# Kernel tuning notes

Measured on AMD Instinct MI355X. Metric: run time of the kernel, lower is better.

The kernel has to match this reference:

```python
import jax, jax.numpy as jnp
import numpy as np

W_LEN = 37  # window_length
EPS = 1e-9
LRELU_SLOPE = 0.2
SQRT2 = 1.4142135623730951


def win_sum(x, w):
    # Depthwise sliding-window sum of width w, 'same' padding w//2 (odd w).
    # Equivalent to the diag-kernel conv1d in the original code, but O(T) via cumsum.
    pad = w // 2
    xp = jnp.pad(x, ((0, 0), (0, 0), (pad, pad)))
    cs = jnp.cumsum(xp, axis=-1)
    cs = jnp.pad(cs, ((0, 0), (0, 0), (1, 0)))
    return cs[..., w:] - cs[..., :-w]


def conv1d(x, w, b):
    # x: [B,C,T], w: [O,I,3], padding=1
    y = jax.lax.conv_general_dilated(x, w, (1,), [(1, 1)],
                                     dimension_numbers=('NCH', 'OIH', 'NCH'))
    return y + b[None, :, None]


def adawin_instance(x, s, mask, fc_w, fc_b, alpha):
    # x: [B,C,T], s: [B,S,T], mask: [B,T]
    C = x.shape[1]
    h = jnp.einsum('bst,cs->bct', s, fc_w) + fc_b[None, :, None]  # [B,2C,T]
    m = mask[:, None, :]                       # [B,1,T]
    denom = win_sum(m, W_LEN) + EPS            # same for all channels
    gamma = win_sum(h[:, :C], W_LEN) / denom * m
    beta = win_sum(h[:, C:], W_LEN) / denom * m
    x_norm = jnp.tanh(alpha * x)               # WindowedNorm1d.forward
    return (1.0 + gamma) * x_norm + beta


def setup_inputs() -> dict:
    key = jax.random.key(0)
    ks = jax.random.split(key, 10)
    B, C_IN, C_OUT, S, T = 16, 512, 512, 128, 2048
    inp = {
        'x': jax.random.normal(ks[0], (B, C_IN, T), dtype=jnp.float32),
        's': jax.random.normal(ks[1], (B, S, T), dtype=jnp.float32),
        'lengths': jax.random.randint(ks[2], (B,), 0, T).astype(jnp.int32),
        'fc1_w': jax.random.normal(ks[3], (2 * C_IN, S), dtype=jnp.float32) * 0.05,
        'fc1_b': jnp.zeros((2 * C_IN,), dtype=jnp.float32),
        'alpha1': jnp.full((1,), 0.5, dtype=jnp.float32),
        'conv1_w': jax.random.normal(ks[4], (C_OUT, C_IN, 3), dtype=jnp.float32) * 0.02,
        'conv1_b': jnp.zeros((C_OUT,), dtype=jnp.float32),
        'fc2_w': jax.random.normal(ks[5], (2 * C_OUT, S), dtype=jnp.float32) * 0.05,
        'fc2_b': jnp.zeros((2 * C_OUT,), dtype=jnp.float32),
        'alpha2': jnp.full((1,), 0.5, dtype=jnp.float32),
        'conv2_w': jax.random.normal(ks[6], (C_OUT, C_OUT, 3), dtype=jnp.float32) * 0.02,
        'conv2_b': jnp.zeros((C_OUT,), dtype=jnp.float32),
    }
    return inp


def reference(x, s, lengths, fc1_w, fc1_b, alpha1, conv1_w, conv1_b,
              fc2_w, fc2_b, alpha2, conv2_w, conv2_b):
    T = x.shape[2]
    mask = (jnp.arange(T)[None, :] < lengths[:, None]).astype(x.dtype)  # [B,T]

    h = adawin_instance(x, s, mask, fc1_w, fc1_b, alpha1)
    h = jax.nn.leaky_relu(h, LRELU_SLOPE)
    h = conv1d(h, conv1_w, conv1_b)
    h = adawin_instance(h, s, mask, fc2_w, fc2_b, alpha2)
    h = jax.nn.leaky_relu(h, LRELU_SLOPE)
    h = conv1d(h, conv2_w, conv2_b)

    # dim_in == dim_out -> identity shortcut
    return (h + x) / SQRT2
```

## Files before the change

### kernel.cpp

```cpp
#include <hip/hip_runtime.h>

#define B_ 16
#define C_ 512
#define S_ 128
#define T_ 2048
#define HALF 18
#define WLEN 37

typedef __bf16 bf16x8 __attribute__((ext_vector_type(8)));
typedef float f32x4 __attribute__((ext_vector_type(4)));
typedef float f32x16 __attribute__((ext_vector_type(16)));
typedef unsigned short ushort_t;

__device__ inline ushort_t f2bf(float x) {
    unsigned u = __float_as_uint(x);
    u += 0x7fffu + ((u >> 16) & 1u);
    return (ushort_t)(u >> 16);
}
__device__ inline float bf2f(ushort_t h) {
    return __uint_as_float(((unsigned)h) << 16);
}

#define MFMA16(a, b, c) __builtin_amdgcn_mfma_f32_16x16x32_bf16((a), (b), (c), 0, 0, 0)
#define MFMA32(a, b, c) __builtin_amdgcn_mfma_f32_32x32x16_bf16((a), (b), (c), 0, 0, 0)

__global__ void prep_weights(const float* __restrict__ fc1, const float* __restrict__ fc2,
                             const float* __restrict__ c1, const float* __restrict__ c2,
                             ushort_t* __restrict__ Wfc, ushort_t* __restrict__ Wc1,
                             ushort_t* __restrict__ Wc2) {
    const int n_fc = 1024 * 128;
    const int n_c = 512 * 1536;
    const int total = 2 * n_fc + 2 * n_c;
    for (int idx = blockIdx.x * blockDim.x + threadIdx.x; idx < total;
         idx += gridDim.x * blockDim.x) {
        if (idx < n_fc) {
            Wfc[idx] = f2bf(fc1[idx]);
        } else if (idx < 2 * n_fc) {
            Wfc[idx] = f2bf(fc2[idx - n_fc]);
        } else {
            int r = idx - 2 * n_fc;
            const float* src = c1;
            ushort_t* dst = Wc1;
            if (r >= n_c) { r -= n_c; src = c2; dst = Wc2; }
            int o = r / 1536;
            int rem = r - o * 1536;
            int k = rem >> 9;
            int i = rem & 511;
            dst[o * 1536 + (k << 9) + i] = f2bf(src[(o * 512 + i) * 3 + k]);
        }
    }
}

__global__ void zero_pads(ushort_t* __restrict__ y1p, ushort_t* __restrict__ y2p) {
    int tid = blockIdx.x * blockDim.x + threadIdx.x;
    if (tid < 4096) {
        ushort_t* base = (tid & 1) ? y2p : y1p;
        int r = tid >> 1;
        int bb = r >> 7;
        int rowsel = (r >> 6) & 1;
        int col = (r & 63) * 8;
        size_t row = (size_t)bb * (T_ + 2) + (rowsel ? (T_ + 1) : 0);
        *(uint4*)&base[row * C_ + col] = (uint4){0, 0, 0, 0};
    }
}

__global__ __launch_bounds__(256) void winsum_kernel(const float* __restrict__ s,
                                                     ushort_t* __restrict__ sw_t) {
    int b = blockIdx.y;
    int t0 = blockIdx.x * 64;
    __shared__ float sb[128][101];
    int tid = threadIdx.x;
    for (int e = tid; e < 128 * 100; e += 256) {
        int sj = e / 100;
        int u = e - sj * 100;
        int gt = t0 - HALF + u;
        float v = 0.f;
        if (gt >= 0 && gt < T_) v = s[((size_t)(b * S_ + sj)) * T_ + gt];
        sb[sj][u] = v;
    }
    __syncthreads();
    for (int e = tid; e < 64 * 128; e += 256) {
        int tl = e >> 7;
        int sj = e & 127;
        float sum = 0.f;
#pragma unroll
        for (int d = 0; d < WLEN; ++d) sum += sb[sj][tl + d];
        sw_t[((size_t)(b * T_ + t0 + tl)) * S_ + sj] = f2bf(sum);
    }
}

template <int INLAYOUT>
__global__ __launch_bounds__(256) void adawin_kernel(
    const void* __restrict__ xin_, const ushort_t* __restrict__ sw_t,
    const ushort_t* __restrict__ Wfc, const float* __restrict__ fcb,
    const float* __restrict__ alpha, const int* __restrict__ lengths,
    ushort_t* __restrict__ youtp) {
    int t0 = blockIdx.x * 64;
    int c0 = blockIdx.y * 64;
    int b = blockIdx.z;
    __shared__ __attribute__((aligned(16))) ushort_t As[128][136];
    __shared__ __attribute__((aligned(16))) ushort_t Bs[64][136];
    int tid = threadIdx.x;

    {
        int r = tid >> 4;
        int cseg = (tid & 15) * 8;
#pragma unroll
        for (int p = 0; p < 8; ++p) {
            int row = p * 16 + r;
            int grow = (row < 64) ? (c0 + row) : (448 + c0 + row);
            *(uint4*)&As[row][cseg] = *(const uint4*)&Wfc[(size_t)grow * 128 + cseg];
        }
    }
    {
        int tl = tid & 63;
        int sg = tid >> 6;
        const ushort_t* src = &sw_t[((size_t)(b * T_ + t0 + tl)) * S_];
#pragma unroll
        for (int j = 0; j < 4; ++j) {
            int col = sg * 32 + j * 8;
            *(uint4*)&Bs[tl][col] = *(const uint4*)&src[col];
        }
    }
    __syncthreads();

    int wave = tid >> 6, lane = tid & 63;
    int quad = lane >> 4, l = lane & 15;
    f32x4 accg[4], accb[4];
#pragma unroll
    for (int n = 0; n < 4; ++n) {
        accg[n] = (f32x4){0.f, 0.f, 0.f, 0.f};
        accb[n] = (f32x4){0.f, 0.f, 0.f, 0.f};
    }
    int rg = wave * 16 + l;
    int rb = 64 + wave * 16 + l;
#pragma unroll
    for (int ks = 0; ks < 4; ++ks) {
        int kc = ks * 32 + quad * 8;
        bf16x8 ag = *(const bf16x8*)&As[rg][kc];
        bf16x8 ab = *(const bf16x8*)&As[rb][kc];
#pragma unroll
        for (int n = 0; n < 4; ++n) {
            bf16x8 bb = *(const bf16x8*)&Bs[n * 16 + l][kc];
            accg[n] = MFMA16(ag, bb, accg[n]);
            accb[n] = MFMA16(ab, bb, accb[n]);
        }
    }

    int len = lengths[b];
    float alph = alpha[0];
    const float* xf = (const float*)xin_;
    const ushort_t* xh = (const ushort_t*)xin_;
    int cbase = c0 + wave * 16 + quad * 4;
#pragma unroll
    for (int n = 0; n < 4; ++n) {
        int t = t0 + n * 16 + l;
        int lo = t - HALF; if (lo < 0) lo = 0;
        int hi = t + HALF; if (hi > T_ - 1) hi = T_ - 1;
        float cnt = (float)(hi - lo + 1);
        int hv = hi < (len - 1) ? hi : (len - 1);
        int mdi = hv - lo + 1; if (mdi < 0) mdi = 0;
        float m = (t < len) ? 1.f : 0.f;
        float sc = m / ((float)mdi + 1e-9f);

        float xv[4];
        if (INLAYOUT == 0) {
#pragma unroll
            for (int j = 0; j < 4; ++j)
                xv[j] = xf[(size_t)(b * C_ + cbase + j) * T_ + t];
        } else {
            uint2 xraw = *(const uint2*)&xh[((size_t)(b * (T_ + 2) + 1 + t)) * C_ + cbase];
            xv[0] = bf2f((ushort_t)(xraw.x & 0xffff));
            xv[1] = bf2f((ushort_t)(xraw.x >> 16));
            xv[2] = bf2f((ushort_t)(xraw.y & 0xffff));
            xv[3] = bf2f((ushort_t)(xraw.y >> 16));
        }
        unsigned pk[2];
#pragma unroll
        for (int j = 0; j < 4; ++j) {
            int c = cbase + j;
            float gamma = (accg[n][j] + fcb[c] * cnt) * sc;
            float beta = (accb[n][j] + fcb[C_ + c] * cnt) * sc;
            float xn = tanhf(alph * xv[j]);
            float v = (1.f + gamma) * xn + beta;
            v = v > 0.f ? v : 0.2f * v;
            unsigned hv16 = (unsigned)f2bf(v);
            if (j & 1) pk[j >> 1] |= hv16 << 16;
            else pk[j >> 1] = hv16;
        }
        *(uint2*)&youtp[((size_t)(b * (T_ + 2) + 1 + t)) * C_ + cbase] =
            (uint2){pk[0], pk[1]};
    }
}

template <int EPI>
__global__ __launch_bounds__(256) void conv_kernel(
    const ushort_t* __restrict__ Xp, const ushort_t* __restrict__ Wc,
    const float* __restrict__ bias, const float* __restrict__ resid,
    ushort_t* __restrict__ out_bf, float* __restrict__ out_f) {
    int t0 = blockIdx.x * 128;
    int o0 = blockIdx.y * 128;
    int b = blockIdx.z;
    __shared__ __attribute__((aligned(16))) ushort_t As[128][104];
    __shared__ __attribute__((aligned(16))) ushort_t Bs[130][56];
    int tid = threadIdx.x;
    int lane = tid & 63, wave = tid >> 6;
    int l32 = lane & 31, khalf = lane >> 5;
    int wo = (wave & 1) * 64, wt = (wave >> 1) * 64;

    f32x16 acc[2][2];
#pragma unroll
    for (int io = 0; io < 2; ++io)
#pragma unroll
        for (int it = 0; it < 2; ++it)
#pragma unroll
            for (int r = 0; r < 16; ++r) acc[io][it][r] = 0.f;

    const ushort_t* xbase = Xp + (size_t)(b * (T_ + 2) + t0) * C_;

#pragma unroll 1
    for (int ch = 0; ch < 16; ++ch) {
        int cb = ch * 32;
#pragma unroll
        for (int p = 0; p < 6; ++p) {
            int e = p * 256 + tid;
            int row = e / 12, seg = e % 12;
            int tap = seg >> 2, kk = (seg & 3) * 8;
            *(uint4*)&As[row][seg * 8] =
                *(const uint4*)&Wc[(size_t)(o0 + row) * 1536 + tap * 512 + cb + kk];
        }
#pragma unroll
        for (int p = 0; p < 3; ++p) {
            int e = p * 256 + tid;
            if (e < 520) {
                int r = e >> 2, seg = e & 3;
                *(uint4*)&Bs[r][seg * 8] = *(const uint4*)&xbase[(size_t)r * C_ + cb + seg * 8];
            }
        }
        __syncthreads();
#pragma unroll
        for (int tap = 0; tap < 3; ++tap) {
#pragma unroll
            for (int ks = 0; ks < 2; ++ks) {
                int kc = tap * 32 + ks * 16 + khalf * 8;
                bf16x8 a0 = *(const bf16x8*)&As[wo + l32][kc];
                bf16x8 a1 = *(const bf16x8*)&As[wo + 32 + l32][kc];
#pragma unroll
                for (int it = 0; it < 2; ++it) {
                    bf16x8 bb =
                        *(const bf16x8*)&Bs[wt + it * 32 + l32 + tap][ks * 16 + khalf * 8];
                    acc[0][it] = MFMA32(a0, bb, acc[0][it]);
                    acc[1][it] = MFMA32(a1, bb, acc[1][it]);
                }
            }
        }
        __syncthreads();
    }

#pragma unroll
    for (int io = 0; io < 2; ++io)
#pragma unroll
        for (int it = 0; it < 2; ++it) {
            int obase = o0 + wo + io * 64 ? 0 : 0;
            obase = o0 + wo + io * 32;
            int t = t0 + wt + it * 32 + l32;
            if (EPI == 0) {
                size_t rowoff = ((size_t)(b * (T_ + 2) + 1 + t)) * C_;
#pragma unroll
                for (int g = 0; g < 4; ++g) {
                    int oo = obase + g * 8 + khalf * 4;
                    unsigned pk[2];
#pragma unroll
                    for (int j = 0; j < 4; ++j) {
                        float v = acc[io][it][g * 4 + j] + bias[oo + j];
                        unsigned hv16 = (unsigned)f2bf(v);
                        if (j & 1) pk[j >> 1] |= hv16 << 16;
                        else pk[j >> 1] = hv16;
                    }
                    *(uint2*)&out_bf[rowoff + oo] = (uint2){pk[0], pk[1]};
                }
            } else {
#pragma unroll
                for (int g = 0; g < 4; ++g) {
                    int oo = obase + g * 8 + khalf * 4;
#pragma unroll
                    for (int j = 0; j < 4; ++j) {
                        size_t off = (size_t)(b * C_ + oo + j) * T_ + t;
                        out_f[off] = (acc[io][it][g * 4 + j] + bias[oo + j] + resid[off]) *
                                     0.70710678118654752f;
                    }
                }
            }
        }
}

extern "C" void kernel_launch(void* const* d_in, const int* in_sizes, int n_in,
                              void* d_out, int out_size, void* d_ws, size_t ws_size,
                              hipStream_t stream) {
    const float* x = (const float*)d_in[0];
    const float* s = (const float*)d_in[1];
    const int* lengths = (const int*)d_in[2];
    const float* fc1_w = (const float*)d_in[3];
    const float* fc1_b = (const float*)d_in[4];
    const float* alpha1 = (const float*)d_in[5];
    const float* conv1_w = (const float*)d_in[6];
    const float* conv1_b = (const float*)d_in[7];
    const float* fc2_w = (const float*)d_in[8];
    const float* fc2_b = (const float*)d_in[9];
    const float* alpha2 = (const float*)d_in[10];
    const float* conv2_w = (const float*)d_in[11];
    const float* conv2_b = (const float*)d_in[12];

    char* ws = (char*)d_ws;
    ushort_t* sw_t = (ushort_t*)ws; ws += (size_t)B_ * T_ * S_ * 2;
    ushort_t* Wfc = (ushort_t*)ws;  ws += (size_t)2 * 1024 * 128 * 2;
    ushort_t* Wc1 = (ushort_t*)ws;  ws += (size_t)512 * 1536 * 2;
    ushort_t* Wc2 = (ushort_t*)ws;  ws += (size_t)512 * 1536 * 2;
    ushort_t* y1p = (ushort_t*)ws;  ws += (size_t)B_ * (T_ + 2) * C_ * 2;
    ushort_t* y2p = (ushort_t*)ws;  ws += (size_t)B_ * (T_ + 2) * C_ * 2;
    if ((size_t)(ws - (char*)d_ws) > ws_size) return;

    prep_weights<<<dim3(1024), dim3(256), 0, stream>>>(fc1_w, fc2_w, conv1_w, conv2_w,
                                                       Wfc, Wc1, Wc2);
    winsum_kernel<<<dim3(32, 16), dim3(256), 0, stream>>>(s, sw_t);
    zero_pads<<<dim3(16), dim3(256), 0, stream>>>(y1p, y2p);
    adawin_kernel<0><<<dim3(32, 8, 16), dim3(256), 0, stream>>>(
        (const void*)x, sw_t, Wfc, fc1_b, alpha1, lengths, y1p);
    conv_kernel<0><<<dim3(16, 4, 16), dim3(256), 0, stream>>>(
        y1p, Wc1, conv1_b, (const float*)nullptr, y2p, (float*)nullptr);
    adawin_kernel<1><<<dim3(32, 8, 16), dim3(256), 0, stream>>>(
        (const void*)y2p, sw_t, Wfc + 1024 * 128, fc2_b, alpha2, lengths, y1p);
    conv_kernel<1><<<dim3(16, 4, 16), dim3(256), 0, stream>>>(
        y1p, Wc2, conv2_b, x, (ushort_t*)nullptr, (float*)d_out);
}
```

Measured before the change: 430.1 us.

## Prefetch conv tiles into registers, stage outputs through LDS, fast tanh

The conv kernel now loads the next K-chunk of weights and activations into registers while the current chunk is used for MFMA, replacing the load-then-compute loop with a register double-buffer. It also sets a minimum-occupancy hint in launch_bounds. Both the adawin and conv bf16 epilogues now stage results in shared memory and write 16-byte coalesced rows instead of scattered 8-byte stores. tanhf is replaced with an exp-based approximation, which saves instructions but may lose accuracy or overflow for large inputs.

```diff
diff --git a/kernel.cpp b/kernel.cpp
--- a/kernel.cpp
+++ b/kernel.cpp
@@ -19,6 +19,10 @@
 }
 __device__ inline float bf2f(ushort_t h) {
     return __uint_as_float(((unsigned)h) << 16);
+}
+__device__ inline float fast_tanh(float z) {
+    float e = __expf(2.f * z);
+    return 1.f - __fdividef(2.f, e + 1.f);
 }
 
 #define MFMA16(a, b, c) __builtin_amdgcn_mfma_f32_16x16x32_bf16((a), (b), (c), 0, 0, 0)
@@ -98,8 +102,9 @@
     int t0 = blockIdx.x * 64;
     int c0 = blockIdx.y * 64;
     int b = blockIdx.z;
-    __shared__ __attribute__((aligned(16))) ushort_t As[128][136];
-    __shared__ __attribute__((aligned(16))) ushort_t Bs[64][136];
+    __shared__ __attribute__((aligned(16))) ushort_t smem[128 * 136 + 64 * 136];
+    ushort_t (*As)[136] = (ushort_t(*)[136])smem;
+    ushort_t (*Bs)[136] = (ushort_t(*)[136])(smem + 128 * 136);
     int tid = threadIdx.x;
 
     {
@@ -147,11 +152,15 @@
         }
     }
 
+    __syncthreads();
+    ushort_t (*Ts)[72] = (ushort_t(*)[72])smem;
+
     int len = lengths[b];
     float alph = alpha[0];
     const float* xf = (const float*)xin_;
     const ushort_t* xh = (const ushort_t*)xin_;
-    int cbase = c0 + wave * 16 + quad * 4;
+    int clocal = wave * 16 + quad * 4;
+    int cbase = c0 + clocal;
 #pragma unroll
     for (int n = 0; n < 4; ++n) {
         int t = t0 + n * 16 + l;
@@ -181,33 +190,67 @@
             int c = cbase + j;
             float gamma = (accg[n][j] + fcb[c] * cnt) * sc;
             float beta = (accb[n][j] + fcb[C_ + c] * cnt) * sc;
-            float xn = tanhf(alph * xv[j]);
+            float xn = fast_tanh(alph * xv[j]);
             float v = (1.f + gamma) * xn + beta;
             v = v > 0.f ? v : 0.2f * v;
             unsigned hv16 = (unsigned)f2bf(v);
             if (j & 1) pk[j >> 1] |= hv16 << 16;
             else pk[j >> 1] = hv16;
         }
-        *(uint2*)&youtp[((size_t)(b * (T_ + 2) + 1 + t)) * C_ + cbase] =
-            (uint2){pk[0], pk[1]};
+        *(uint2*)&Ts[n * 16 + l][clocal] = (uint2){pk[0], pk[1]};
+    }
+    __syncthreads();
+    {
+        int row = tid >> 2;
+        int seg = (tid & 3) * 16;
+        size_t gbase = ((size_t)(b * (T_ + 2) + 1 + t0 + row)) * C_ + c0 + seg;
+        *(uint4*)&youtp[gbase] = *(const uint4*)&Ts[row][seg];
+        *(uint4*)&youtp[gbase + 8] = *(const uint4*)&Ts[row][seg + 8];
     }
 }
 
 template <int EPI>
-__global__ __launch_bounds__(256) void conv_kernel(
+__global__ __launch_bounds__(256, 3) void conv_kernel(
     const ushort_t* __restrict__ Xp, const ushort_t* __restrict__ Wc,
     const float* __restrict__ bias, const float* __restrict__ resid,
     ushort_t* __restrict__ out_bf, float* __restrict__ out_f) {
     int t0 = blockIdx.x * 128;
     int o0 = blockIdx.y * 128;
     int b = blockIdx.z;
-    __shared__ __attribute__((aligned(16))) ushort_t As[128][104];
-    __shared__ __attribute__((aligned(16))) ushort_t Bs[130][56];
+    __shared__ __attribute__((aligned(16))) ushort_t smem[128 * 104 + 130 * 56];
+    ushort_t (*As)[104] = (ushort_t(*)[104])smem;
+    ushort_t (*Bs)[56] = (ushort_t(*)[56])(smem + 128 * 104);
     int tid = threadIdx.x;
     int lane = tid & 63, wave = tid >> 6;
     int l32 = lane & 31, khalf = lane >> 5;
     int wo = (wave & 1) * 64, wt = (wave >> 1) * 64;
 
+    const int soE[6] = {0, 8, 16, 24, 512, 520};
+    const int soO[6] = {528, 536, 1024, 1032, 1040, 1048};
+    int odd = tid & 1;
+    int arow = tid >> 1;
+    const ushort_t* abase = Wc + (size_t)(o0 + arow) * 1536;
+    const ushort_t* ap[6];
+    ushort_t* al[6];
+#pragma unroll
+    for (int p = 0; p < 6; ++p) {
+        ap[p] = abase + (odd ? soO[p] : soE[p]);
+        al[p] = &As[arow][odd * 48 + p * 8];
+    }
+    const ushort_t* xbase = Xp + (size_t)(b * (T_ + 2) + t0) * C_;
+    const ushort_t* bp01 = xbase + (size_t)(tid >> 1) * C_ + odd * 16;
+    ushort_t* bl01 = &Bs[tid >> 1][odd * 16];
+    const ushort_t* bp2 = xbase + (size_t)(128 + (tid >> 2)) * C_ + (tid & 3) * 8;
+    ushort_t* bl2 = &Bs[128 + (tid >> 2)][(tid & 3) * 8];
+    bool tail = tid < 8;
+
+    uint4 ra[6], rbv[2], rt;
+#pragma unroll
+    for (int p = 0; p < 6; ++p) ra[p] = *(const uint4*)ap[p];
+#pragma unroll
+    for (int p = 0; p < 2; ++p) rbv[p] = *(const uint4*)(bp01 + p * 8);
+    if (tail) rt = *(const uint4*)bp2;
+
     f32x16 acc[2][2];
 #pragma unroll
     for (int io = 0; io < 2; ++io)
@@ -215,29 +258,24 @@
         for (int it = 0; it < 2; ++it)
 #pragma unroll
             for (int r = 0; r < 16; ++r) acc[io][it][r] = 0.f;
-
-    const ushort_t* xbase = Xp + (size_t)(b * (T_ + 2) + t0) * C_;
 
 #pragma unroll 1
     for (int ch = 0; ch < 16; ++ch) {
-        int cb = ch * 32;
-#pragma unroll
-        for (int p = 0; p < 6; ++p) {
-            int e = p * 256 + tid;
-            int row = e / 12, seg = e % 12;
-            int tap = seg >> 2, kk = (seg & 3) * 8;
-            *(uint4*)&As[row][seg * 8] =
-                *(const uint4*)&Wc[(size_t)(o0 + row) * 1536 + tap * 512 + cb + kk];
-        }
-#pragma unroll
-        for (int p = 0; p < 3; ++p) {
-            int e = p * 256 + tid;
-            if (e < 520) {
-                int r = e >> 2, seg = e & 3;
-                *(uint4*)&Bs[r][seg * 8] = *(const uint4*)&xbase[(size_t)r * C_ + cb + seg * 8];
-            }
-        }
         __syncthreads();
+#pragma unroll
+        for (int p = 0; p < 6; ++p) *(uint4*)al[p] = ra[p];
+#pragma unroll
+        for (int p = 0; p < 2; ++p) *(uint4*)(bl01 + p * 8) = rbv[p];
+        if (tail) *(uint4*)bl2 = rt;
+        __syncthreads();
+        if (ch < 15) {
+            int off = (ch + 1) * 32;
+#pragma unroll
+            for (int p = 0; p < 6; ++p) ra[p] = *(const uint4*)(ap[p] + off);
+#pragma unroll
+            for (int p = 0; p < 2; ++p) rbv[p] = *(const uint4*)(bp01 + off + p * 8);
+            if (tail) rt = *(const uint4*)(bp2 + off);
+        }
 #pragma unroll
         for (int tap = 0; tap < 3; ++tap) {
 #pragma unroll
@@ -254,32 +292,46 @@
                 }
             }
         }
+    }
+
+    if (EPI == 0) {
+        ushort_t (*Ts)[136] = (ushort_t(*)[136])smem;
         __syncthreads();
-    }
-
-#pragma unroll
-    for (int io = 0; io < 2; ++io)
-#pragma unroll
-        for (int it = 0; it < 2; ++it) {
-            int obase = o0 + wo + io * 64 ? 0 : 0;
-            obase = o0 + wo + io * 32;
-            int t = t0 + wt + it * 32 + l32;
-            if (EPI == 0) {
-                size_t rowoff = ((size_t)(b * (T_ + 2) + 1 + t)) * C_;
+#pragma unroll
+        for (int io = 0; io < 2; ++io)
+#pragma unroll
+            for (int it = 0; it < 2; ++it) {
+                int trow = wt + it * 32 + l32;
 #pragma unroll
                 for (int g = 0; g < 4; ++g) {
-                    int oo = obase + g * 8 + khalf * 4;
+                    int oc = wo + io * 32 + g * 8 + khalf * 4;
                     unsigned pk[2];
 #pragma unroll
                     for (int j = 0; j < 4; ++j) {
-                        float v = acc[io][it][g * 4 + j] + bias[oo + j];
+                        float v = acc[io][it][g * 4 + j] + bias[o0 + oc + j];
                         unsigned hv16 = (unsigned)f2bf(v);
                         if (j & 1) pk[j >> 1] |= hv16 << 16;
                         else pk[j >> 1] = hv16;
                     }
-                    *(uint2*)&out_bf[rowoff + oo] = (uint2){pk[0], pk[1]};
+                    *(uint2*)&Ts[trow][oc] = (uint2){pk[0], pk[1]};
                 }
-            } else {
+            }
+        __syncthreads();
+        int cc = (tid & 15) * 8;
+        int rbse = tid >> 4;
+#pragma unroll
+        for (int j = 0; j < 8; ++j) {
+            int row = j * 16 + rbse;
+            *(uint4*)&out_bf[((size_t)(b * (T_ + 2) + 1 + t0 + row)) * C_ + o0 + cc] =
+                *(const uint4*)&Ts[row][cc];
+        }
+    } else {
+#pragma unroll
+        for (int io = 0; io < 2; ++io)
+#pragma unroll
+            for (int it = 0; it < 2; ++it) {
+                int obase = o0 + wo + io * 32;
+                int t = t0 + wt + it * 32 + l32;
 #pragma unroll
                 for (int g = 0; g < 4; ++g) {
                     int oo = obase + g * 8 + khalf * 4;
@@ -291,7 +343,7 @@
                     }
                 }
             }
-        }
+    }
 }
 
 extern "C" void kernel_launch(void* const* d_in, const int* in_sizes, int n_in,
```

New measurement: 596.7 us. +38.8%, slower.
